# Kernel optimization log

Measured on AMD Instinct MI355X. Metric: run time of the kernel, lower is better.

The kernel has to match this reference:

```python
import jax, jax.numpy as jnp
import numpy as np

MODEL_DIMS = 1024
NUM_LAYERS = 4
NUM_SUPPORT = 256


def setup_inputs() -> dict:
    key = jax.random.key(0)
    kx, kk, kv = jax.random.split(key, 3)
    x = jax.random.normal(kx, (4, 4096, MODEL_DIMS), dtype=jnp.float32)
    # Stacked per-layer parameters, matching nn.Parameter(torch.randn(...))
    keys = jax.random.normal(kk, (NUM_LAYERS, NUM_SUPPORT, MODEL_DIMS), dtype=jnp.float32)
    values = jax.random.normal(kv, (NUM_LAYERS, NUM_SUPPORT, MODEL_DIMS), dtype=jnp.float32)
    return {"x": x, "keys": keys, "values": values}


def reference(x, keys, values):
    # Chain of CleanUpKV layers: normalize -> scores -> softmax -> weighted values.
    def step(h, kv):
        k, v = kv  # k, v: [num_support, D]
        hn = h / (jnp.linalg.norm(h, axis=-1, keepdims=True) + 1e-9)
        scores = jnp.einsum('bsd,nd->bsn', hn, k)          # [B,S,num_support]
        w = jax.nn.softmax(scores, axis=-1)
        return jnp.einsum('bsn,nd->bsd', w, v), None

    out, _ = jax.lax.scan(step, x, (keys, values))
    return out
```

## Files before the change

### kernel.cpp

```cpp
#include <hip/hip_runtime.h>
#include <hip/hip_bf16.h>
#include <stdint.h>

#define D 1024
#define NSUP 256
#define ROWS 16384
#define MB 64
#define LTHREADS 1024
#define LGRID (ROWS / MB)
#define LDS_BYTES 163840

typedef __attribute__((__ext_vector_type__(8))) __bf16 bf16x8;
typedef __attribute__((__ext_vector_type__(4))) float f32x4;

#define MFMA16(a, b, c) __builtin_amdgcn_mfma_f32_16x16x32_bf16((a), (b), (c), 0, 0, 0)

__global__ void cast_k_kernel(const float* __restrict__ K, __bf16* __restrict__ Kb) {
    int i = (blockIdx.x * 256 + threadIdx.x) * 4;
    float4 v = *(const float4*)(K + i);
    __bf16 o[4] __attribute__((aligned(8)));
    o[0] = (__bf16)v.x; o[1] = (__bf16)v.y; o[2] = (__bf16)v.z; o[3] = (__bf16)v.w;
    *(uint2*)(Kb + i) = *(const uint2*)o;
}

__global__ void transpose_v_kernel(const float* __restrict__ V, __bf16* __restrict__ Vt) {
    __shared__ __bf16 tile[64][72];
    int l = blockIdx.z;
    int d0 = blockIdx.x * 64, n0 = blockIdx.y * 64;
    const float* Vl = V + (size_t)l * NSUP * D;
    __bf16* Vtl = Vt + (size_t)l * D * NSUP;
    for (int j = 0; j < 16; ++j) {
        int idx = j * 256 + threadIdx.x;
        int n_l = idx >> 6, d_l = idx & 63;
        tile[d_l][n_l] = (__bf16)Vl[(size_t)(n0 + n_l) * D + d0 + d_l];
    }
    __syncthreads();
    for (int j = 0; j < 16; ++j) {
        int idx = j * 256 + threadIdx.x;
        int d_l = idx >> 6, n_l = idx & 63;
        Vtl[(size_t)(d0 + d_l) * NSUP + n0 + n_l] = tile[d_l][n_l];
    }
}

__global__ void __launch_bounds__(LTHREADS) __attribute__((amdgpu_waves_per_eu(4, 4)))
fused4_kernel(const float* __restrict__ x, float* __restrict__ out,
              const __bf16* __restrict__ Kb, const __bf16* __restrict__ Vt) {
    extern __shared__ __align__(16) char pool[];
    char* wbuf = pool + 131072;
    const int tid = threadIdx.x;
    const int lane = tid & 63;
    const int wv = tid >> 6;
    const int llo = lane & 15, lhi = lane >> 4;
    const int swzk = (llo & 7) << 4;
    const int row0 = blockIdx.x * MB;

    {
        const int srow = tid >> 4, c16 = tid & 15;
        const float* xr = x + (size_t)(row0 + srow) * D;
        const int sk = (srow & 7) << 4;
        float ss = 0.f;
        #pragma unroll
        for (int q = 0; q < 16; ++q) {
            float4 v = *(const float4*)(xr + (c16 + q * 16) * 4);
            ss += v.x * v.x + v.y * v.y + v.z * v.z + v.w * v.w;
            __bf16 t[4] __attribute__((aligned(8)));
            t[0] = (__bf16)v.x; t[1] = (__bf16)v.y; t[2] = (__bf16)v.z; t[3] = (__bf16)v.w;
            *(uint2*)(pool + srow * 2048 + (((c16 + q * 16) * 8) ^ sk)) = *(const uint2*)t;
        }
        ss += __shfl_xor(ss, 1); ss += __shfl_xor(ss, 2);
        ss += __shfl_xor(ss, 4); ss += __shfl_xor(ss, 8);
        if (c16 == 0) *(float*)(wbuf + srow * 4) = 1.f / (sqrtf(ss) + 1e-9f);
    }
    __syncthreads();

    float sqp[4][4];

    #pragma unroll 1
    for (int l = 0; l < 4; ++l) {
        if (l > 0) {
            #pragma unroll
            for (int rf = 0; rf < 4; ++rf)
                #pragma unroll
                for (int r = 0; r < 4; ++r)
                    if (llo == 0)
                        *(float*)(wbuf + (rf * 16 + lhi * 4 + r) * 64 + wv * 4) = sqp[rf][r];
        }

        f32x4 acc[4];
        #pragma unroll
        for (int rf = 0; rf < 4; ++rf) acc[rf] = (f32x4){0.f, 0.f, 0.f, 0.f};
        const __bf16* kb0 = Kb + (size_t)l * NSUP * D + (size_t)(wv * 16 + llo) * D + lhi * 8;
        bf16x8 kbuf[2][4];
        #pragma unroll
        for (int j = 0; j < 4; ++j) kbuf[0][j] = *(const bf16x8*)(kb0 + j * 32);
        #pragma unroll
        for (int kc = 0; kc < 8; ++kc) {
            if (kc < 7) {
                #pragma unroll
                for (int j = 0; j < 4; ++j)
                    kbuf[(kc + 1) & 1][j] = *(const bf16x8*)(kb0 + ((kc + 1) * 4 + j) * 32);
            }
            #pragma unroll
            for (int j = 0; j < 4; ++j) {
                const int k = kc * 4 + j;
                #pragma unroll
                for (int rf = 0; rf < 4; ++rf) {
                    bf16x8 a = *(const bf16x8*)(pool + (rf * 16 + llo) * 2048
                                                + ((k * 64 + lhi * 16) ^ swzk));
                    acc[rf] = MFMA16(a, kbuf[kc & 1][j], acc[rf]);
                }
            }
        }
        __syncthreads();

        float rnv[4][4];
        if (l == 0) {
            #pragma unroll
            for (int rf = 0; rf < 4; ++rf)
                #pragma unroll
                for (int r = 0; r < 4; ++r)
                    rnv[rf][r] = *(const float*)(wbuf + (rf * 16 + lhi * 4 + r) * 4);
        } else {
            #pragma unroll
            for (int rf = 0; rf < 4; ++rf)
                #pragma unroll
                for (int r = 0; r < 4; ++r) {
                    const f32x4* rp = (const f32x4*)(wbuf + (rf * 16 + lhi * 4 + r) * 64);
                    f32x4 s0 = rp[0], s1 = rp[1], s2 = rp[2], s3 = rp[3];
                    float ss = (s0[0] + s0[1] + s0[2] + s0[3]) + (s1[0] + s1[1] + s1[2] + s1[3])
                             + (s2[0] + s2[1] + s2[2] + s2[3]) + (s3[0] + s3[1] + s3[2] + s3[3]);
                    rnv[rf][r] = 1.f / (sqrtf(ss) + 1e-9f);
                }
        }

        float ee[4][4];
        #pragma unroll
        for (int rf = 0; rf < 4; ++rf)
            #pragma unroll
            for (int r = 0; r < 4; ++r) {
                float e = exp2f(acc[rf][r] * rnv[rf][r] * 1.44269504f);
                ee[rf][r] = e;
                float s = e;
                s += __shfl_xor(s, 1); s += __shfl_xor(s, 2);
                s += __shfl_xor(s, 4); s += __shfl_xor(s, 8);
                if (llo == 0) *(float*)(pool + (rf * 16 + lhi * 4 + r) * 64 + wv * 4) = s;
            }
        __syncthreads();

        #pragma unroll
        for (int rf = 0; rf < 4; ++rf)
            #pragma unroll
            for (int r = 0; r < 4; ++r) {
                int row = rf * 16 + lhi * 4 + r;
                const f32x4* rp = (const f32x4*)(pool + row * 64);
                f32x4 s0 = rp[0], s1 = rp[1], s2 = rp[2], s3 = rp[3];
                float S = (s0[0] + s0[1] + s0[2] + s0[3]) + (s1[0] + s1[1] + s1[2] + s1[3])
                        + (s2[0] + s2[1] + s2[2] + s2[3]) + (s3[0] + s3[1] + s3[2] + s3[3]);
                float inv = 1.f / S;
                *(__bf16*)(wbuf + row * 512 + (((wv * 16 + llo) * 2) ^ ((row & 7) << 4))) =
                    (__bf16)(ee[rf][r] * inv);
            }
        __syncthreads();

        float sql[4][4];
        #pragma unroll
        for (int rf = 0; rf < 4; ++rf)
            #pragma unroll
            for (int r = 0; r < 4; ++r) sql[rf][r] = 0.f;

        #pragma unroll 1
        for (int cfh = 0; cfh < 2; ++cfh) {
            f32x4 acc2[4][2];
            #pragma unroll
            for (int rf = 0; rf < 4; ++rf)
                #pragma unroll
                for (int c2 = 0; c2 < 2; ++c2)
                    acc2[rf][c2] = (f32x4){0.f, 0.f, 0.f, 0.f};
            const __bf16* vt0 = Vt + (size_t)l * D * NSUP
                              + (size_t)(wv * 64 + cfh * 32 + llo) * NSUP + lhi * 8;
            bf16x8 vbuf[2][2];
            #pragma unroll
            for (int c2 = 0; c2 < 2; ++c2)
                vbuf[0][c2] = *(const bf16x8*)(vt0 + (size_t)c2 * 16 * NSUP);
            #pragma unroll
            for (int k = 0; k < 8; ++k) {
                if (k < 7) {
                    #pragma unroll
                    for (int c2 = 0; c2 < 2; ++c2)
                        vbuf[(k + 1) & 1][c2] = *(const bf16x8*)(vt0 + (size_t)c2 * 16 * NSUP + (k + 1) * 32);
                }
                bf16x8 a[4];
                #pragma unroll
                for (int rf = 0; rf < 4; ++rf)
                    a[rf] = *(const bf16x8*)(wbuf + (rf * 16 + llo) * 512
                                             + ((k * 64 + lhi * 16) ^ swzk));
                #pragma unroll
                for (int c2 = 0; c2 < 2; ++c2)
                    #pragma unroll
                    for (int rf = 0; rf < 4; ++rf)
                        acc2[rf][c2] = MFMA16(a[rf], vbuf[k & 1][c2], acc2[rf][c2]);
            }
            if (l < 3) {
                #pragma unroll
                for (int rf = 0; rf < 4; ++rf)
                    #pragma unroll
                    for (int c2 = 0; c2 < 2; ++c2)
                        #pragma unroll
                        for (int r = 0; r < 4; ++r) {
                            int row = rf * 16 + lhi * 4 + r;
                            int col = wv * 64 + cfh * 32 + c2 * 16 + llo;
                            float v = acc2[rf][c2][r];
                            *(__bf16*)(pool + row * 2048 + ((col * 2) ^ ((row & 7) << 4))) = (__bf16)v;
                            sql[rf][r] += v * v;
                        }
            } else {
                #pragma unroll
                for (int rf = 0; rf < 4; ++rf)
                    #pragma unroll
                    for (int c2 = 0; c2 < 2; ++c2)
                        #pragma unroll
                        for (int r = 0; r < 4; ++r) {
                            int row = rf * 16 + lhi * 4 + r;
                            int col = wv * 64 + cfh * 32 + c2 * 16 + llo;
                            out[(size_t)(row0 + row) * D + col] = acc2[rf][c2][r];
                        }
            }
        }

        if (l < 3) {
            #pragma unroll
            for (int rf = 0; rf < 4; ++rf)
                #pragma unroll
                for (int r = 0; r < 4; ++r) {
                    float s = sql[rf][r];
                    s += __shfl_xor(s, 1); s += __shfl_xor(s, 2);
                    s += __shfl_xor(s, 4); s += __shfl_xor(s, 8);
                    sqp[rf][r] = s;
                }
            __syncthreads();
        }
    }
}

extern "C" void kernel_launch(void* const* d_in, const int* in_sizes, int n_in,
                              void* d_out, int out_size, void* d_ws, size_t ws_size,
                              hipStream_t stream) {
    const float* x = (const float*)d_in[0];
    const float* keys = (const float*)d_in[1];
    const float* values = (const float*)d_in[2];
    float* out = (float*)d_out;

    char* ws = (char*)d_ws;
    __bf16* Kb = (__bf16*)(ws);
    __bf16* Vt = (__bf16*)(ws + 2097152);

    (void)hipFuncSetAttribute((const void*)fused4_kernel,
                              hipFuncAttributeMaxDynamicSharedMemorySize, LDS_BYTES);

    cast_k_kernel<<<1024, 256, 0, stream>>>(keys, Kb);
    transpose_v_kernel<<<dim3(16, 4, 4), 256, 0, stream>>>(values, Vt);
    fused4_kernel<<<LGRID, LTHREADS, LDS_BYTES, stream>>>(x, out, Kb, Vt);
}
```

Before: 260.2 us.

## Halve row tile to 32 rows with 8 waves and retile MFMA work

Shrinks each block from 64 rows with 16 waves to 32 rows with 8 waves, halving LDS use so more blocks can be resident per CU, and doubles the grid. Each wave now computes 32 support columns for the score GEMM and 128 output columns for the value GEMM, so the per-wave MFMA tiling and the softmax and norm reductions are reshaped to match. The waves_per_eu hint is dropped. In exchange, K and V fragments are reused across fewer rows per block, which raises global/L2 traffic for the weights.

```diff
diff --git a/kernel.cpp b/kernel.cpp
--- a/kernel.cpp
+++ b/kernel.cpp
@@ -5,10 +5,10 @@
 #define D 1024
 #define NSUP 256
 #define ROWS 16384
-#define MB 64
-#define LTHREADS 1024
+#define MB 32
+#define LTHREADS 512
 #define LGRID (ROWS / MB)
-#define LDS_BYTES 163840
+#define LDS_BYTES 81920
 
 typedef __attribute__((__ext_vector_type__(8))) __bf16 bf16x8;
 typedef __attribute__((__ext_vector_type__(4))) float f32x4;
@@ -42,11 +42,11 @@
     }
 }
 
-__global__ void __launch_bounds__(LTHREADS) __attribute__((amdgpu_waves_per_eu(4, 4)))
+__global__ void __launch_bounds__(LTHREADS)
 fused4_kernel(const float* __restrict__ x, float* __restrict__ out,
               const __bf16* __restrict__ Kb, const __bf16* __restrict__ Vt) {
     extern __shared__ __align__(16) char pool[];
-    char* wbuf = pool + 131072;
+    char* wbuf = pool + 65536;
     const int tid = threadIdx.x;
     const int lane = tid & 63;
     const int wv = tid >> 6;
@@ -73,111 +73,116 @@
     }
     __syncthreads();
 
-    float sqp[4][4];
+    float sqp[2][4];
 
     #pragma unroll 1
     for (int l = 0; l < 4; ++l) {
         if (l > 0) {
             #pragma unroll
-            for (int rf = 0; rf < 4; ++rf)
+            for (int rf = 0; rf < 2; ++rf)
                 #pragma unroll
                 for (int r = 0; r < 4; ++r)
                     if (llo == 0)
-                        *(float*)(wbuf + (rf * 16 + lhi * 4 + r) * 64 + wv * 4) = sqp[rf][r];
-        }
-
-        f32x4 acc[4];
-        #pragma unroll
-        for (int rf = 0; rf < 4; ++rf) acc[rf] = (f32x4){0.f, 0.f, 0.f, 0.f};
-        const __bf16* kb0 = Kb + (size_t)l * NSUP * D + (size_t)(wv * 16 + llo) * D + lhi * 8;
-        bf16x8 kbuf[2][4];
-        #pragma unroll
-        for (int j = 0; j < 4; ++j) kbuf[0][j] = *(const bf16x8*)(kb0 + j * 32);
-        #pragma unroll
-        for (int kc = 0; kc < 8; ++kc) {
-            if (kc < 7) {
-                #pragma unroll
-                for (int j = 0; j < 4; ++j)
-                    kbuf[(kc + 1) & 1][j] = *(const bf16x8*)(kb0 + ((kc + 1) * 4 + j) * 32);
-            }
-            #pragma unroll
-            for (int j = 0; j < 4; ++j) {
-                const int k = kc * 4 + j;
-                #pragma unroll
-                for (int rf = 0; rf < 4; ++rf) {
-                    bf16x8 a = *(const bf16x8*)(pool + (rf * 16 + llo) * 2048
-                                                + ((k * 64 + lhi * 16) ^ swzk));
-                    acc[rf] = MFMA16(a, kbuf[kc & 1][j], acc[rf]);
-                }
+                        *(float*)(wbuf + (rf * 16 + lhi * 4 + r) * 32 + wv * 4) = sqp[rf][r];
+        }
+
+        f32x4 acc[2][2];
+        #pragma unroll
+        for (int rf = 0; rf < 2; ++rf)
+            #pragma unroll
+            for (int cf = 0; cf < 2; ++cf)
+                acc[rf][cf] = (f32x4){0.f, 0.f, 0.f, 0.f};
+        const __bf16* kb0 = Kb + (size_t)l * NSUP * D + (size_t)(wv * 32 + llo) * D + lhi * 8;
+        bf16x8 kbuf[2][2];
+        #pragma unroll
+        for (int cf = 0; cf < 2; ++cf)
+            kbuf[0][cf] = *(const bf16x8*)(kb0 + (size_t)cf * 16 * D);
+        #pragma unroll
+        for (int k = 0; k < 32; ++k) {
+            if (k < 31) {
+                #pragma unroll
+                for (int cf = 0; cf < 2; ++cf)
+                    kbuf[(k + 1) & 1][cf] = *(const bf16x8*)(kb0 + (size_t)cf * 16 * D + (k + 1) * 32);
+            }
+            bf16x8 a0 = *(const bf16x8*)(pool + llo * 2048 + ((k * 64 + lhi * 16) ^ swzk));
+            bf16x8 a1 = *(const bf16x8*)(pool + (16 + llo) * 2048 + ((k * 64 + lhi * 16) ^ swzk));
+            #pragma unroll
+            for (int cf = 0; cf < 2; ++cf) {
+                acc[0][cf] = MFMA16(a0, kbuf[k & 1][cf], acc[0][cf]);
+                acc[1][cf] = MFMA16(a1, kbuf[k & 1][cf], acc[1][cf]);
             }
         }
         __syncthreads();
 
-        float rnv[4][4];
+        float rnv[2][4];
         if (l == 0) {
             #pragma unroll
-            for (int rf = 0; rf < 4; ++rf)
+            for (int rf = 0; rf < 2; ++rf)
                 #pragma unroll
                 for (int r = 0; r < 4; ++r)
                     rnv[rf][r] = *(const float*)(wbuf + (rf * 16 + lhi * 4 + r) * 4);
         } else {
             #pragma unroll
-            for (int rf = 0; rf < 4; ++rf)
+            for (int rf = 0; rf < 2; ++rf)
                 #pragma unroll
                 for (int r = 0; r < 4; ++r) {
-                    const f32x4* rp = (const f32x4*)(wbuf + (rf * 16 + lhi * 4 + r) * 64);
-                    f32x4 s0 = rp[0], s1 = rp[1], s2 = rp[2], s3 = rp[3];
-                    float ss = (s0[0] + s0[1] + s0[2] + s0[3]) + (s1[0] + s1[1] + s1[2] + s1[3])
-                             + (s2[0] + s2[1] + s2[2] + s2[3]) + (s3[0] + s3[1] + s3[2] + s3[3]);
+                    const f32x4* rp = (const f32x4*)(wbuf + (rf * 16 + lhi * 4 + r) * 32);
+                    f32x4 s0 = rp[0], s1 = rp[1];
+                    float ss = (s0[0] + s0[1] + s0[2] + s0[3]) + (s1[0] + s1[1] + s1[2] + s1[3]);
                     rnv[rf][r] = 1.f / (sqrtf(ss) + 1e-9f);
                 }
         }
 
-        float ee[4][4];
-        #pragma unroll
-        for (int rf = 0; rf < 4; ++rf)
+        float ee[2][2][4];
+        #pragma unroll
+        for (int rf = 0; rf < 2; ++rf)
             #pragma unroll
             for (int r = 0; r < 4; ++r) {
-                float e = exp2f(acc[rf][r] * rnv[rf][r] * 1.44269504f);
-                ee[rf][r] = e;
-                float s = e;
+                float sc = rnv[rf][r] * 1.44269504f;
+                float e0 = exp2f(acc[rf][0][r] * sc);
+                float e1 = exp2f(acc[rf][1][r] * sc);
+                ee[rf][0][r] = e0; ee[rf][1][r] = e1;
+                float s = e0 + e1;
                 s += __shfl_xor(s, 1); s += __shfl_xor(s, 2);
                 s += __shfl_xor(s, 4); s += __shfl_xor(s, 8);
-                if (llo == 0) *(float*)(pool + (rf * 16 + lhi * 4 + r) * 64 + wv * 4) = s;
+                if (llo == 0) *(float*)(pool + (rf * 16 + lhi * 4 + r) * 32 + wv * 4) = s;
             }
         __syncthreads();
 
         #pragma unroll
-        for (int rf = 0; rf < 4; ++rf)
+        for (int rf = 0; rf < 2; ++rf)
             #pragma unroll
             for (int r = 0; r < 4; ++r) {
                 int row = rf * 16 + lhi * 4 + r;
-                const f32x4* rp = (const f32x4*)(pool + row * 64);
-                f32x4 s0 = rp[0], s1 = rp[1], s2 = rp[2], s3 = rp[3];
-                float S = (s0[0] + s0[1] + s0[2] + s0[3]) + (s1[0] + s1[1] + s1[2] + s1[3])
-                        + (s2[0] + s2[1] + s2[2] + s2[3]) + (s3[0] + s3[1] + s3[2] + s3[3]);
+                const f32x4* rp = (const f32x4*)(pool + row * 32);
+                f32x4 s0 = rp[0], s1 = rp[1];
+                float S = (s0[0] + s0[1] + s0[2] + s0[3]) + (s1[0] + s1[1] + s1[2] + s1[3]);
                 float inv = 1.f / S;
-                *(__bf16*)(wbuf + row * 512 + (((wv * 16 + llo) * 2) ^ ((row & 7) << 4))) =
-                    (__bf16)(ee[rf][r] * inv);
+                #pragma unroll
+                for (int cf = 0; cf < 2; ++cf) {
+                    int col = wv * 32 + cf * 16 + llo;
+                    *(__bf16*)(wbuf + row * 512 + ((col * 2) ^ ((row & 7) << 4))) =
+                        (__bf16)(ee[rf][cf][r] * inv);
+                }
             }
         __syncthreads();
 
-        float sql[4][4];
-        #pragma unroll
-        for (int rf = 0; rf < 4; ++rf)
+        float sql[2][4];
+        #pragma unroll
+        for (int rf = 0; rf < 2; ++rf)
             #pragma unroll
             for (int r = 0; r < 4; ++r) sql[rf][r] = 0.f;
 
         #pragma unroll 1
-        for (int cfh = 0; cfh < 2; ++cfh) {
-            f32x4 acc2[4][2];
-            #pragma unroll
-            for (int rf = 0; rf < 4; ++rf)
+        for (int ch = 0; ch < 4; ++ch) {
+            f32x4 acc2[2][2];
+            #pragma unroll
+            for (int rf = 0; rf < 2; ++rf)
                 #pragma unroll
                 for (int c2 = 0; c2 < 2; ++c2)
                     acc2[rf][c2] = (f32x4){0.f, 0.f, 0.f, 0.f};
             const __bf16* vt0 = Vt + (size_t)l * D * NSUP
-                              + (size_t)(wv * 64 + cfh * 32 + llo) * NSUP + lhi * 8;
+                              + (size_t)(wv * 128 + ch * 32 + llo) * NSUP + lhi * 8;
             bf16x8 vbuf[2][2];
             #pragma unroll
             for (int c2 = 0; c2 < 2; ++c2)
@@ -189,39 +194,36 @@
                     for (int c2 = 0; c2 < 2; ++c2)
                         vbuf[(k + 1) & 1][c2] = *(const bf16x8*)(vt0 + (size_t)c2 * 16 * NSUP + (k + 1) * 32);
                 }
-                bf16x8 a[4];
-                #pragma unroll
-                for (int rf = 0; rf < 4; ++rf)
-                    a[rf] = *(const bf16x8*)(wbuf + (rf * 16 + llo) * 512
-                                             + ((k * 64 + lhi * 16) ^ swzk));
-                #pragma unroll
-                for (int c2 = 0; c2 < 2; ++c2)
-                    #pragma unroll
-                    for (int rf = 0; rf < 4; ++rf)
-                        acc2[rf][c2] = MFMA16(a[rf], vbuf[k & 1][c2], acc2[rf][c2]);
+                bf16x8 a0 = *(const bf16x8*)(wbuf + llo * 512 + ((k * 64 + lhi * 16) ^ swzk));
+                bf16x8 a1 = *(const bf16x8*)(wbuf + (16 + llo) * 512 + ((k * 64 + lhi * 16) ^ swzk));
+                #pragma unroll
+                for (int c2 = 0; c2 < 2; ++c2) {
+                    acc2[0][c2] = MFMA16(a0, vbuf[k & 1][c2], acc2[0][c2]);
+                    acc2[1][c2] = MFMA16(a1, vbuf[k & 1][c2], acc2[1][c2]);
+                }
             }
             if (l < 3) {
                 #pragma unroll
-                for (int rf = 0; rf < 4; ++rf)
+                for (int rf = 0; rf < 2; ++rf)
                     #pragma unroll
                     for (int c2 = 0; c2 < 2; ++c2)
                         #pragma unroll
                         for (int r = 0; r < 4; ++r) {
                             int row = rf * 16 + lhi * 4 + r;
-                            int col = wv * 64 + cfh * 32 + c2 * 16 + llo;
+                            int col = wv * 128 + ch * 32 + c2 * 16 + llo;
                             float v = acc2[rf][c2][r];
                             *(__bf16*)(pool + row * 2048 + ((col * 2) ^ ((row & 7) << 4))) = (__bf16)v;
                             sql[rf][r] += v * v;
                         }
             } else {
                 #pragma unroll
-                for (int rf = 0; rf < 4; ++rf)
+                for (int rf = 0; rf < 2; ++rf)
                     #pragma unroll
                     for (int c2 = 0; c2 < 2; ++c2)
                         #pragma unroll
                         for (int r = 0; r < 4; ++r) {
                             int row = rf * 16 + lhi * 4 + r;
-                            int col = wv * 64 + cfh * 32 + c2 * 16 + llo;
+                            int col = wv * 128 + ch * 32 + c2 * 16 + llo;
                             out[(size_t)(row0 + row) * D + col] = acc2[rf][c2][r];
                         }
             }
@@ -229,7 +231,7 @@
 
         if (l < 3) {
             #pragma unroll
-            for (int rf = 0; rf < 4; ++rf)
+            for (int rf = 0; rf < 2; ++rf)
                 #pragma unroll
                 for (int r = 0; r < 4; ++r) {
                     float s = sql[rf][r];
```

Measured after the change: 318.3 us. 1.22x slower.

## Shrink LDS footprint by overlaying softmax weights on activation buffer, recompute norms from bf16

Applied to the files above, without the earlier changes.

Drops the separate 32KB weight buffer and places the softmax weights inside the activation pool at offset 98304, cutting LDS from 160KB to 128KB. Rows 48-63 of the next-layer activations would overlap the weights, so their bf16 values are held in registers and written back after a barrier. Row norms are now recomputed each layer from the bf16 activations in LDS instead of being accumulated from fp32 outputs, which slightly changes precision. The K loop becomes a flat 4-deep register prefetch, the V loop works on 16-column chunks, and the waves_per_eu pin is removed, which may change register allocation.

```diff
diff --git a/kernel.cpp b/kernel.cpp
--- a/kernel.cpp
+++ b/kernel.cpp
@@ -8,12 +8,22 @@
 #define MB 64
 #define LTHREADS 1024
 #define LGRID (ROWS / MB)
-#define LDS_BYTES 163840
+#define LDS_BYTES 131072
+#define WBASE 98304
 
 typedef __attribute__((__ext_vector_type__(8))) __bf16 bf16x8;
 typedef __attribute__((__ext_vector_type__(4))) float f32x4;
+typedef __attribute__((__ext_vector_type__(4))) uint32_t u32x4;
 
 #define MFMA16(a, b, c) __builtin_amdgcn_mfma_f32_16x16x32_bf16((a), (b), (c), 0, 0, 0)
+
+static __device__ __forceinline__ float bb2f(uint32_t b) {
+    union { uint32_t u; float f; } c; c.u = b; return c.f;
+}
+static __device__ __forceinline__ uint32_t bfbits(float f) {
+    __bf16 b = (__bf16)f;
+    return (uint32_t)*(uint16_t*)&b;
+}
 
 __global__ void cast_k_kernel(const float* __restrict__ K, __bf16* __restrict__ Kb) {
     int i = (blockIdx.x * 256 + threadIdx.x) * 4;
@@ -42,11 +52,11 @@
     }
 }
 
-__global__ void __launch_bounds__(LTHREADS) __attribute__((amdgpu_waves_per_eu(4, 4)))
+__global__ void __launch_bounds__(LTHREADS)
 fused4_kernel(const float* __restrict__ x, float* __restrict__ out,
               const __bf16* __restrict__ Kb, const __bf16* __restrict__ Vt) {
     extern __shared__ __align__(16) char pool[];
-    char* wbuf = pool + 131072;
+    __shared__ float rnred[MB];
     const int tid = threadIdx.x;
     const int lane = tid & 63;
     const int wv = tid >> 6;
@@ -58,92 +68,69 @@
         const int srow = tid >> 4, c16 = tid & 15;
         const float* xr = x + (size_t)(row0 + srow) * D;
         const int sk = (srow & 7) << 4;
-        float ss = 0.f;
         #pragma unroll
         for (int q = 0; q < 16; ++q) {
             float4 v = *(const float4*)(xr + (c16 + q * 16) * 4);
-            ss += v.x * v.x + v.y * v.y + v.z * v.z + v.w * v.w;
             __bf16 t[4] __attribute__((aligned(8)));
             t[0] = (__bf16)v.x; t[1] = (__bf16)v.y; t[2] = (__bf16)v.z; t[3] = (__bf16)v.w;
             *(uint2*)(pool + srow * 2048 + (((c16 + q * 16) * 8) ^ sk)) = *(const uint2*)t;
         }
-        ss += __shfl_xor(ss, 1); ss += __shfl_xor(ss, 2);
-        ss += __shfl_xor(ss, 4); ss += __shfl_xor(ss, 8);
-        if (c16 == 0) *(float*)(wbuf + srow * 4) = 1.f / (sqrtf(ss) + 1e-9f);
     }
     __syncthreads();
-
-    float sqp[4][4];
 
     #pragma unroll 1
     for (int l = 0; l < 4; ++l) {
-        if (l > 0) {
-            #pragma unroll
-            for (int rf = 0; rf < 4; ++rf)
-                #pragma unroll
-                for (int r = 0; r < 4; ++r)
-                    if (llo == 0)
-                        *(float*)(wbuf + (rf * 16 + lhi * 4 + r) * 64 + wv * 4) = sqp[rf][r];
+        #pragma unroll
+        for (int rr = 0; rr < 4; ++rr) {
+            int row = wv * 4 + rr;
+            const char* rb = pool + row * 2048;
+            int key = (row & 7) << 4;
+            float s = 0.f;
+            #pragma unroll
+            for (int h2 = 0; h2 < 2; ++h2) {
+                u32x4 u = *(const u32x4*)(rb + ((lane * 32 + h2 * 16) ^ key));
+                #pragma unroll
+                for (int j = 0; j < 4; ++j) {
+                    float f0 = bb2f(u[j] << 16), f1 = bb2f(u[j] & 0xffff0000u);
+                    s += f0 * f0 + f1 * f1;
+                }
+            }
+            s += __shfl_xor(s, 1); s += __shfl_xor(s, 2); s += __shfl_xor(s, 4);
+            s += __shfl_xor(s, 8); s += __shfl_xor(s, 16); s += __shfl_xor(s, 32);
+            if (lane == 0) rnred[row] = s;
         }
 
         f32x4 acc[4];
         #pragma unroll
         for (int rf = 0; rf < 4; ++rf) acc[rf] = (f32x4){0.f, 0.f, 0.f, 0.f};
         const __bf16* kb0 = Kb + (size_t)l * NSUP * D + (size_t)(wv * 16 + llo) * D + lhi * 8;
-        bf16x8 kbuf[2][4];
-        #pragma unroll
-        for (int j = 0; j < 4; ++j) kbuf[0][j] = *(const bf16x8*)(kb0 + j * 32);
-        #pragma unroll
-        for (int kc = 0; kc < 8; ++kc) {
-            if (kc < 7) {
-                #pragma unroll
-                for (int j = 0; j < 4; ++j)
-                    kbuf[(kc + 1) & 1][j] = *(const bf16x8*)(kb0 + ((kc + 1) * 4 + j) * 32);
-            }
-            #pragma unroll
-            for (int j = 0; j < 4; ++j) {
-                const int k = kc * 4 + j;
-                #pragma unroll
-                for (int rf = 0; rf < 4; ++rf) {
-                    bf16x8 a = *(const bf16x8*)(pool + (rf * 16 + llo) * 2048
-                                                + ((k * 64 + lhi * 16) ^ swzk));
-                    acc[rf] = MFMA16(a, kbuf[kc & 1][j], acc[rf]);
-                }
+        bf16x8 kb[4];
+        #pragma unroll
+        for (int p = 0; p < 3; ++p) kb[p] = *(const bf16x8*)(kb0 + p * 32);
+        #pragma unroll
+        for (int k = 0; k < 32; ++k) {
+            if (k < 29) kb[(k + 3) & 3] = *(const bf16x8*)(kb0 + (k + 3) * 32);
+            #pragma unroll
+            for (int rf = 0; rf < 4; ++rf) {
+                bf16x8 a = *(const bf16x8*)(pool + (rf * 16 + llo) * 2048
+                                            + ((k * 64 + lhi * 16) ^ swzk));
+                acc[rf] = MFMA16(a, kb[k & 3], acc[rf]);
             }
         }
         __syncthreads();
 
-        float rnv[4][4];
-        if (l == 0) {
-            #pragma unroll
-            for (int rf = 0; rf < 4; ++rf)
-                #pragma unroll
-                for (int r = 0; r < 4; ++r)
-                    rnv[rf][r] = *(const float*)(wbuf + (rf * 16 + lhi * 4 + r) * 4);
-        } else {
-            #pragma unroll
-            for (int rf = 0; rf < 4; ++rf)
-                #pragma unroll
-                for (int r = 0; r < 4; ++r) {
-                    const f32x4* rp = (const f32x4*)(wbuf + (rf * 16 + lhi * 4 + r) * 64);
-                    f32x4 s0 = rp[0], s1 = rp[1], s2 = rp[2], s3 = rp[3];
-                    float ss = (s0[0] + s0[1] + s0[2] + s0[3]) + (s1[0] + s1[1] + s1[2] + s1[3])
-                             + (s2[0] + s2[1] + s2[2] + s2[3]) + (s3[0] + s3[1] + s3[2] + s3[3]);
-                    rnv[rf][r] = 1.f / (sqrtf(ss) + 1e-9f);
-                }
-        }
-
-        float ee[4][4];
         #pragma unroll
         for (int rf = 0; rf < 4; ++rf)
             #pragma unroll
             for (int r = 0; r < 4; ++r) {
-                float e = exp2f(acc[rf][r] * rnv[rf][r] * 1.44269504f);
-                ee[rf][r] = e;
+                int row = rf * 16 + lhi * 4 + r;
+                float rn = 1.f / (sqrtf(rnred[row]) + 1e-9f);
+                float e = exp2f(acc[rf][r] * rn * 1.44269504f);
+                acc[rf][r] = e;
                 float s = e;
                 s += __shfl_xor(s, 1); s += __shfl_xor(s, 2);
                 s += __shfl_xor(s, 4); s += __shfl_xor(s, 8);
-                if (llo == 0) *(float*)(pool + (rf * 16 + lhi * 4 + r) * 64 + wv * 4) = s;
+                if (llo == 0) *(float*)(pool + row * 64 + wv * 4) = s;
             }
         __syncthreads();
 
@@ -157,86 +144,72 @@
                 float S = (s0[0] + s0[1] + s0[2] + s0[3]) + (s1[0] + s1[1] + s1[2] + s1[3])
                         + (s2[0] + s2[1] + s2[2] + s2[3]) + (s3[0] + s3[1] + s3[2] + s3[3]);
                 float inv = 1.f / S;
-                *(__bf16*)(wbuf + row * 512 + (((wv * 16 + llo) * 2) ^ ((row & 7) << 4))) =
-                    (__bf16)(ee[rf][r] * inv);
+                int col = wv * 16 + llo;
+                *(__bf16*)(pool + WBASE + row * 512 + ((col * 2) ^ ((row & 7) << 4))) =
+                    (__bf16)(acc[rf][r] * inv);
             }
         __syncthreads();
 
-        float sql[4][4];
-        #pragma unroll
-        for (int rf = 0; rf < 4; ++rf)
-            #pragma unroll
-            for (int r = 0; r < 4; ++r) sql[rf][r] = 0.f;
-
-        #pragma unroll 1
-        for (int cfh = 0; cfh < 2; ++cfh) {
-            f32x4 acc2[4][2];
-            #pragma unroll
-            for (int rf = 0; rf < 4; ++rf)
-                #pragma unroll
-                for (int c2 = 0; c2 < 2; ++c2)
-                    acc2[rf][c2] = (f32x4){0.f, 0.f, 0.f, 0.f};
+        uint32_t def[4][2];
+        #pragma unroll
+        for (int ch = 0; ch < 4; ++ch) {
+            f32x4 acc2[4];
+            #pragma unroll
+            for (int rf = 0; rf < 4; ++rf) acc2[rf] = (f32x4){0.f, 0.f, 0.f, 0.f};
             const __bf16* vt0 = Vt + (size_t)l * D * NSUP
-                              + (size_t)(wv * 64 + cfh * 32 + llo) * NSUP + lhi * 8;
-            bf16x8 vbuf[2][2];
-            #pragma unroll
-            for (int c2 = 0; c2 < 2; ++c2)
-                vbuf[0][c2] = *(const bf16x8*)(vt0 + (size_t)c2 * 16 * NSUP);
+                              + (size_t)(wv * 64 + ch * 16 + llo) * NSUP + lhi * 8;
+            bf16x8 vb[4];
+            #pragma unroll
+            for (int p = 0; p < 3; ++p) vb[p] = *(const bf16x8*)(vt0 + p * 32);
             #pragma unroll
             for (int k = 0; k < 8; ++k) {
-                if (k < 7) {
+                if (k < 5) vb[(k + 3) & 3] = *(const bf16x8*)(vt0 + (k + 3) * 32);
+                #pragma unroll
+                for (int rf = 0; rf < 4; ++rf) {
+                    bf16x8 aw = *(const bf16x8*)(pool + WBASE + (rf * 16 + llo) * 512
+                                                 + ((k * 64 + lhi * 16) ^ swzk));
+                    acc2[rf] = MFMA16(aw, vb[k & 3], acc2[rf]);
+                }
+            }
+            int col = wv * 64 + ch * 16 + llo;
+            if (l < 3) {
+                #pragma unroll
+                for (int rf = 0; rf < 3; ++rf)
                     #pragma unroll
-                    for (int c2 = 0; c2 < 2; ++c2)
-                        vbuf[(k + 1) & 1][c2] = *(const bf16x8*)(vt0 + (size_t)c2 * 16 * NSUP + (k + 1) * 32);
-                }
-                bf16x8 a[4];
-                #pragma unroll
-                for (int rf = 0; rf < 4; ++rf)
-                    a[rf] = *(const bf16x8*)(wbuf + (rf * 16 + llo) * 512
-                                             + ((k * 64 + lhi * 16) ^ swzk));
-                #pragma unroll
-                for (int c2 = 0; c2 < 2; ++c2)
-                    #pragma unroll
-                    for (int rf = 0; rf < 4; ++rf)
-                        acc2[rf][c2] = MFMA16(a[rf], vbuf[k & 1][c2], acc2[rf][c2]);
-            }
-            if (l < 3) {
+                    for (int r = 0; r < 4; ++r) {
+                        int row = rf * 16 + lhi * 4 + r;
+                        *(__bf16*)(pool + row * 2048 + ((col * 2) ^ ((row & 7) << 4))) =
+                            (__bf16)acc2[rf][r];
+                    }
+                def[ch][0] = bfbits(acc2[3][0]) | (bfbits(acc2[3][1]) << 16);
+                def[ch][1] = bfbits(acc2[3][2]) | (bfbits(acc2[3][3]) << 16);
+            } else {
                 #pragma unroll
                 for (int rf = 0; rf < 4; ++rf)
                     #pragma unroll
-                    for (int c2 = 0; c2 < 2; ++c2)
-                        #pragma unroll
-                        for (int r = 0; r < 4; ++r) {
-                            int row = rf * 16 + lhi * 4 + r;
-                            int col = wv * 64 + cfh * 32 + c2 * 16 + llo;
-                            float v = acc2[rf][c2][r];
-                            *(__bf16*)(pool + row * 2048 + ((col * 2) ^ ((row & 7) << 4))) = (__bf16)v;
-                            sql[rf][r] += v * v;
-                        }
-            } else {
-                #pragma unroll
-                for (int rf = 0; rf < 4; ++rf)
-                    #pragma unroll
-                    for (int c2 = 0; c2 < 2; ++c2)
-                        #pragma unroll
-                        for (int r = 0; r < 4; ++r) {
-                            int row = rf * 16 + lhi * 4 + r;
-                            int col = wv * 64 + cfh * 32 + c2 * 16 + llo;
-                            out[(size_t)(row0 + row) * D + col] = acc2[rf][c2][r];
-                        }
+                    for (int r = 0; r < 4; ++r) {
+                        int row = rf * 16 + lhi * 4 + r;
+                        out[(size_t)(row0 + row) * D + col] = acc2[rf][r];
+                    }
             }
         }
 
         if (l < 3) {
-            #pragma unroll
-            for (int rf = 0; rf < 4; ++rf)
-                #pragma unroll
-                for (int r = 0; r < 4; ++r) {
-                    float s = sql[rf][r];
-                    s += __shfl_xor(s, 1); s += __shfl_xor(s, 2);
-                    s += __shfl_xor(s, 4); s += __shfl_xor(s, 8);
-                    sqp[rf][r] = s;
+            __syncthreads();
+            #pragma unroll
+            for (int ch = 0; ch < 4; ++ch) {
+                int col = wv * 64 + ch * 16 + llo;
+                #pragma unroll
+                for (int rp = 0; rp < 2; ++rp) {
+                    uint32_t pk = def[ch][rp];
+                    int re = 48 + lhi * 4 + rp * 2;
+                    int ro = re + 1;
+                    *(uint16_t*)(pool + re * 2048 + ((col * 2) ^ ((re & 7) << 4))) =
+                        (uint16_t)(pk & 0xffff);
+                    *(uint16_t*)(pool + ro * 2048 + ((col * 2) ^ ((ro & 7) << 4))) =
+                        (uint16_t)(pk >> 16);
                 }
+            }
             __syncthreads();
         }
     }
```

After: 593.7 us. +128.1%, slower.
